# Optimization experiments

Measured on AMD Instinct MI355X. Metric: run time of the kernel, lower is better.

The kernel has to match this reference:

```python
import jax, jax.numpy as jnp
import numpy as np

WS = 7          # window size (square)
SS = 3          # shift size
NH = 6          # num heads
EPS = 1e-5      # LayerNorm eps (torch default)


def _ln(x, g, b):
    m = jnp.mean(x, axis=-1, keepdims=True)
    v = jnp.mean(jnp.square(x - m), axis=-1, keepdims=True)
    return (x - m) * jax.lax.rsqrt(v + EPS) * g + b


def _window_partition(x):
    # (B,H,W,C) -> (B*nW, WS*WS, C)
    B, H, W, C = x.shape
    x = x.reshape(B, H // WS, WS, W // WS, WS, C)
    return x.transpose(0, 1, 3, 2, 4, 5).reshape(-1, WS * WS, C)


def _window_reverse(w, B, H, W):
    C = w.shape[-1]
    x = w.reshape(B, H // WS, W // WS, WS, WS, C)
    return x.transpose(0, 1, 3, 2, 4, 5).reshape(B, H, W, C)


def _make_rpi():
    coords = np.stack(np.meshgrid(np.arange(WS), np.arange(WS), indexing='ij'))  # (2,WS,WS)
    cf = coords.reshape(2, -1)
    rel = cf[:, :, None] - cf[:, None, :]            # (2,N,N)
    rel = rel.transpose(1, 2, 0).astype(np.int64)
    rel[..., 0] += WS - 1
    rel[..., 1] += WS - 1
    rel[..., 0] *= 2 * WS - 1
    return rel.sum(-1)                               # (N,N)


def _make_mask(H, W):
    # standard shifted-window attention mask, values in {0, -100}
    img = np.zeros((H, W), dtype=np.float32)
    cnt = 0
    for hs in (slice(0, -WS), slice(-WS, -SS), slice(-SS, None)):
        for ws_ in (slice(0, -WS), slice(-WS, -SS), slice(-SS, None)):
            img[hs, ws_] = cnt
            cnt += 1
    win = img.reshape(H // WS, WS, W // WS, WS).transpose(0, 2, 1, 3).reshape(-1, WS * WS)
    diff = win[:, None, :] - win[:, :, None]
    return np.where(diff != 0, np.float32(-100.0), np.float32(0.0))  # (nW,N,N)


def setup_inputs() -> dict:
    key = jax.random.key(0)
    ks = jax.random.split(key, 8)
    B, H, W, C = 16, 112, 112, 192
    Dh = C * 4
    s = 0.02
    inp = {
        'x': jax.random.normal(ks[0], (B, H, W, C), jnp.float32),
        'mask_matrix': jnp.asarray(_make_mask(H, W)),
        'rpi': jnp.asarray(_make_rpi(), jnp.int32),
        'rpb_table': s * jax.random.normal(ks[1], ((2 * WS - 1) ** 2, NH), jnp.float32),
        'norm1_g': jnp.ones((C,), jnp.float32),
        'norm1_b': jnp.zeros((C,), jnp.float32),
        'qkv_w': s * jax.random.normal(ks[2], (3 * C, C), jnp.float32),
        'qkv_b': jnp.zeros((3 * C,), jnp.float32),
        'proj_w': s * jax.random.normal(ks[3], (C, C), jnp.float32),
        'proj_b': jnp.zeros((C,), jnp.float32),
        'norm2_g': jnp.ones((C,), jnp.float32),
        'norm2_b': jnp.zeros((C,), jnp.float32),
        'fc1_w': s * jax.random.normal(ks[4], (Dh, C), jnp.float32),
        'fc1_b': jnp.zeros((Dh,), jnp.float32),
        'fc2_w': s * jax.random.normal(ks[5], (C, Dh), jnp.float32),
        'fc2_b': jnp.zeros((C,), jnp.float32),
    }
    return inp


def reference(x, mask_matrix, rpi, rpb_table, norm1_g, norm1_b, qkv_w, qkv_b,
              proj_w, proj_b, norm2_g, norm2_b, fc1_w, fc1_b, fc2_w, fc2_b):
    B, H, W, C = x.shape
    N = WS * WS
    hd = C // NH
    scale = hd ** -0.5

    shortcut = x
    xn = _ln(x, norm1_g, norm1_b)
    shifted = jnp.roll(xn, shift=(-SS, -SS), axis=(1, 2))

    xw = _window_partition(shifted)                          # (B_, N, C)
    B_ = xw.shape[0]
    qkv = xw @ qkv_w.T + qkv_b                               # (B_, N, 3C)
    qkv = qkv.reshape(B_, N, 3, NH, hd).transpose(2, 0, 3, 1, 4)
    q, k, v = qkv[0] * scale, qkv[1], qkv[2]                 # (B_, NH, N, hd)

    attn = jnp.einsum('bhnd,bhmd->bhnm', q, k)               # (B_, NH, N, N)
    bias = rpb_table[rpi.reshape(-1)].reshape(N, N, NH).transpose(2, 0, 1)
    attn = attn + bias[None]

    nW = mask_matrix.shape[0]
    attn = attn.reshape(B_ // nW, nW, NH, N, N) + mask_matrix[None, :, None]
    attn = jax.nn.softmax(attn.reshape(B_, NH, N, N), axis=-1)

    out = jnp.einsum('bhnm,bhmd->bhnd', attn, v)             # (B_, NH, N, hd)
    out = out.transpose(0, 2, 1, 3).reshape(B_, N, C)
    out = out @ proj_w.T + proj_b

    shifted = _window_reverse(out, B, H, W)
    xa = jnp.roll(shifted, shift=(SS, SS), axis=(1, 2))
    x = shortcut + xa

    h = _ln(x, norm2_g, norm2_b)
    h = jax.nn.gelu(h @ fc1_w.T + fc1_b, approximate=False)
    h = h @ fc2_w.T + fc2_b
    return x + h
```

## Files before the change

### kernel.cpp

```cpp
#include <hip/hip_runtime.h>
#include <hip/hip_bf16.h>

typedef __hip_bfloat16 bf16;
typedef __attribute__((ext_vector_type(8))) short bh8;
typedef __attribute__((ext_vector_type(4))) short bh4;
typedef __attribute__((ext_vector_type(4))) float f4;

#define TOKENS 200704
#define CDIM   192

__device__ __forceinline__ void gload16(const bf16* g, bf16* l) {
    __builtin_amdgcn_global_load_lds((const __attribute__((address_space(1))) void*)g,
                                     (__attribute__((address_space(3))) void*)l,
                                     16, 0, 0);
}
#define MFMA __builtin_amdgcn_mfma_f32_16x16x32_bf16

__device__ __forceinline__ void stv(float* p, float v) { *p = v; }
__device__ __forceinline__ void stv(bf16* p, float v)  { *p = __float2bfloat16(v); }
__device__ __forceinline__ short f2bs(float v) {
    bf16 h = __float2bfloat16(v); return *(short*)&h;
}

__device__ __forceinline__ int row2tok(int row) {
    int win = row / 49, n = row - win * 49;
    int b = win >> 8, rem = win & 255;
    int hs = (rem >> 4) * 7 + n / 7;
    int wsx = (rem & 15) * 7 + n % 7;
    int hh = hs + 3; if (hh >= 112) hh -= 112;
    int ww = wsx + 3; if (ww >= 112) ww -= 112;
    return (b * 112 + hh) * 112 + ww;
}

__global__ void cvt_all(const float* __restrict__ a, const float* __restrict__ b,
                        const float* __restrict__ c, const float* __restrict__ d,
                        bf16* __restrict__ dst) {
    int i = blockIdx.x * 256 + threadIdx.x;
    if (i >= 442368) return;
    float v;
    if (i < 110592)       v = a[i];
    else if (i < 147456)  v = b[i - 110592];
    else if (i < 294912)  v = c[i - 147456];
    else                  v = d[i - 294912];
    dst[i] = __float2bfloat16(v);
}

__global__ void bmp_kernel(const int* __restrict__ rpi, const float* __restrict__ tab,
                           const float* __restrict__ mask, float* __restrict__ bmp) {
    int idx = blockIdx.x * 256 + threadIdx.x;
    if (idx >= 98304) return;
    int cls = idx / 24576, rem = idx - cls * 24576;
    int h = rem >> 12, qk = rem & 4095;
    int qq = qk >> 6, kk = qk & 63;
    float v;
    if (kk >= 49) v = -1e30f;
    else if (qq >= 49) v = 0.f;
    else {
        int rep = ((cls & 2) ? 240 : 0) + ((cls & 1) ? 15 : 0);
        v = tab[rpi[qq * 49 + kk] * 6 + h] + mask[rep * 2401 + qq * 49 + kk];
    }
    bmp[idx] = v;
}

template<int GATHER>
__global__ __launch_bounds__(256)
void ln_kernel(const float* __restrict__ src, const float* __restrict__ gw,
               const float* __restrict__ bw, bf16* __restrict__ dst) {
    const int lane = threadIdx.x & 63;
    const int gwv  = (blockIdx.x * 256 + threadIdx.x) >> 6;
    const int nwv  = (gridDim.x * 256) >> 6;
    const float g0 = gw[lane], g1 = gw[lane + 64], g2 = gw[lane + 128];
    const float b0 = bw[lane], b1 = bw[lane + 64], b2 = bw[lane + 128];
    for (int row = gwv; row < TOKENS; row += nwv) {
        const float* p = GATHER ? src + (size_t)row2tok(row) * CDIM
                                : src + (size_t)row * CDIM;
        float v0 = p[lane], v1 = p[lane + 64], v2 = p[lane + 128];
        float s = v0 + v1 + v2;
        float q = v0 * v0 + v1 * v1 + v2 * v2;
        #pragma unroll
        for (int o = 32; o; o >>= 1) { s += __shfl_xor(s, o, 64); q += __shfl_xor(q, o, 64); }
        float mean = s * (1.f / 192.f);
        float var  = q * (1.f / 192.f) - mean * mean;
        float rstd = rsqrtf(var + 1e-5f);
        bf16* d = dst + (size_t)row * CDIM;
        d[lane]       = __float2bfloat16((v0 - mean) * rstd * g0 + b0);
        d[lane + 64]  = __float2bfloat16((v1 - mean) * rstd * g1 + b1);
        d[lane + 128] = __float2bfloat16((v2 - mean) * rstd * g2 + b2);
    }
}

template<int EPI, int FUSELN, typename OutT>
__global__ __launch_bounds__(256)
void gemm_bt(const bf16* __restrict__ A, const bf16* __restrict__ W,
             const float* __restrict__ bias, OutT* out,
             const float* res, int N, int K,
             const float* __restrict__ g2, const float* __restrict__ b2g,
             bf16* __restrict__ hbuf) {
    __shared__ __align__(16) bf16 As[128 * 32];
    __shared__ __align__(16) bf16 Bs[192 * 32];
    __shared__ float rsum[FUSELN ? 128 : 1][2], rsq[FUSELN ? 128 : 1][2];
    const int tid = threadIdx.x, wid = tid >> 6, lane = tid & 63;
    const int mbase = blockIdx.y * 128, nbase = blockIdx.x * 192;
    const int wm = wid >> 1, wn = wid & 1;
    const int r = lane & 15, q = lane >> 4;
    const int sx = (q ^ ((r >> 1) & 3)) << 3;
    const bf16* Ab = A + (size_t)mbase * K;
    const bf16* Wb = W + (size_t)nbase * K;
    f4 acc[4][6] = {};
    const int cbase = wid * 64 + lane;
    for (int k0 = 0; k0 < K; k0 += 32) {
        #pragma unroll
        for (int p = 0; p < 2; ++p) {
            int ci = p * 256 + cbase;
            int row = ci >> 2, g = (ci & 3) ^ ((row >> 1) & 3);
            gload16(Ab + (size_t)row * K + (k0 + (g << 3)),
                    &As[(p * 256 + wid * 64) * 8]);
        }
        #pragma unroll
        for (int p = 0; p < 3; ++p) {
            int ci = p * 256 + cbase;
            int row = ci >> 2, g = (ci & 3) ^ ((row >> 1) & 3);
            gload16(Wb + (size_t)row * K + (k0 + (g << 3)),
                    &Bs[(p * 256 + wid * 64) * 8]);
        }
        __syncthreads();
        bh8 af[4], bfr[6];
        #pragma unroll
        for (int i = 0; i < 4; ++i)
            af[i] = *(const bh8*)&As[(wm * 64 + i * 16 + r) * 32 + sx];
        #pragma unroll
        for (int j = 0; j < 6; ++j)
            bfr[j] = *(const bh8*)&Bs[(wn * 96 + j * 16 + r) * 32 + sx];
        #pragma unroll
        for (int i = 0; i < 4; ++i)
            #pragma unroll
            for (int j = 0; j < 6; ++j)
                acc[i][j] = MFMA(af[i], bfr[j], acc[i][j], 0, 0, 0);
        __syncthreads();
    }
    const int cr = q, cc = r;
    if constexpr (EPI == 0) {
        #pragma unroll
        for (int i = 0; i < 4; ++i)
            #pragma unroll
            for (int j = 0; j < 6; ++j) {
                int ncol = nbase + wn * 96 + j * 16 + cc;
                float bv = bias[ncol];
                #pragma unroll
                for (int rr = 0; rr < 4; ++rr) {
                    int row = mbase + wm * 64 + i * 16 + cr * 4 + rr;
                    stv(&out[(size_t)row * N + ncol], acc[i][j][rr] + bv);
                }
            }
    } else {
        #pragma unroll
        for (int i = 0; i < 4; ++i) {
            size_t dstRow[4];
            float ps[4], pq[4];
            #pragma unroll
            for (int rr = 0; rr < 4; ++rr) {
                int row = mbase + wm * 64 + i * 16 + cr * 4 + rr;
                dstRow[rr] = (size_t)row2tok(row) * CDIM;
                ps[rr] = 0.f; pq[rr] = 0.f;
            }
            #pragma unroll
            for (int j = 0; j < 6; ++j) {
                int ncol = nbase + wn * 96 + j * 16 + cc;
                float bv = bias[ncol];
                #pragma unroll
                for (int rr = 0; rr < 4; ++rr) {
                    float v = acc[i][j][rr] + bv + res[dstRow[rr] + ncol];
                    stv(&out[dstRow[rr] + ncol], v);
                    acc[i][j][rr] = v;
                    ps[rr] += v; pq[rr] += v * v;
                }
            }
            if constexpr (FUSELN) {
                #pragma unroll
                for (int rr = 0; rr < 4; ++rr) {
                    float s = ps[rr], qq = pq[rr];
                    #pragma unroll
                    for (int o = 1; o < 16; o <<= 1) { s += __shfl_xor(s, o, 64); qq += __shfl_xor(qq, o, 64); }
                    if (cc == 0) {
                        int rl = wm * 64 + i * 16 + cr * 4 + rr;
                        rsum[rl][wn] = s; rsq[rl][wn] = qq;
                    }
                }
            }
        }
        if constexpr (FUSELN) {
            __syncthreads();
            #pragma unroll
            for (int i = 0; i < 4; ++i) {
                size_t dstRow[4];
                float mean[4], rstd[4];
                #pragma unroll
                for (int rr = 0; rr < 4; ++rr) {
                    int rl = wm * 64 + i * 16 + cr * 4 + rr;
                    dstRow[rr] = (size_t)row2tok(mbase + rl) * CDIM;
                    float m = (rsum[rl][0] + rsum[rl][1]) * (1.f / 192.f);
                    float var = (rsq[rl][0] + rsq[rl][1]) * (1.f / 192.f) - m * m;
                    mean[rr] = m; rstd[rr] = rsqrtf(var + 1e-5f);
                }
                #pragma unroll
                for (int j = 0; j < 6; ++j) {
                    int ncol = nbase + wn * 96 + j * 16 + cc;
                    float gv = g2[ncol], bvv = b2g[ncol];
                    #pragma unroll
                    for (int rr = 0; rr < 4; ++rr)
                        hbuf[dstRow[rr] + ncol] =
                            __float2bfloat16((acc[i][j][rr] - mean[rr]) * rstd[rr] * gv + bvv);
                }
            }
        }
    }
}

__global__ __launch_bounds__(384, 2)
void qkvattn_kernel(const bf16* __restrict__ xw, const bf16* __restrict__ wq,
                    const float* __restrict__ qkvb, const float* __restrict__ bmp,
                    bf16* __restrict__ attno) {
    __shared__ __align__(16) bf16 xsf[6][64][32];
    __shared__ __align__(16) bf16 qk[6][2][64][32];
    const int tid = threadIdx.x, h = tid >> 6, lane = tid & 63;
    const int r = lane & 15, q = lane >> 4;
    const int win = blockIdx.x;
    const int sxk = (q ^ ((r >> 1) & 3)) << 3;

    #pragma unroll
    for (int it = 0; it < 4; ++it) {
        int l = it * 384 + tid;
        int ks = l >> 8, rem = l & 255, tok = rem >> 2;
        int kg = (rem & 3) ^ ((tok >> 1) & 3);
        int srow = win * 49 + tok; if (srow > 200703) srow = 200703;
        gload16(xw + (size_t)srow * 192 + ks * 32 + kg * 8,
                &xsf[0][0][0] + (size_t)l * 8);
    }
    const bf16* wqh = wq + (size_t)(h * 32 + r) * 192 + q * 8;
    bh8 wqk[4], wv[2];
    #pragma unroll
    for (int i = 0; i < 4; ++i)
        wqk[i] = *(const bh8*)(wqh + (size_t)((i >> 1) * 192 + (i & 1) * 16) * 192);
    #pragma unroll
    for (int jv = 0; jv < 2; ++jv)
        wv[jv] = *(const bh8*)(wqh + (size_t)(384 + jv * 16) * 192);
    __syncthreads();
    f4 aqk[4][4] = {}, av[4][2] = {};
    #pragma unroll
    for (int ks = 0; ks < 6; ++ks) {
        bh8 nqk[4], nv[2];
        if (ks < 5) {
            #pragma unroll
            for (int i = 0; i < 4; ++i)
                nqk[i] = *(const bh8*)(wqh + (size_t)((i >> 1) * 192 + (i & 1) * 16) * 192 + (ks + 1) * 32);
            #pragma unroll
            for (int jv = 0; jv < 2; ++jv)
                nv[jv] = *(const bh8*)(wqh + (size_t)(384 + jv * 16) * 192 + (ks + 1) * 32);
        }
        bh8 xf[4];
        #pragma unroll
        for (int mt = 0; mt < 4; ++mt)
            xf[mt] = *(const bh8*)&xsf[ks][mt * 16 + r][sxk];
        #pragma unroll
        for (int i = 0; i < 4; ++i)
            #pragma unroll
            for (int jn = 0; jn < 4; ++jn)
                aqk[i][jn] = MFMA(wqk[i], xf[jn], aqk[i][jn], 0, 0, 0);
        #pragma unroll
        for (int mt = 0; mt < 4; ++mt)
            #pragma unroll
            for (int jv = 0; jv < 2; ++jv)
                av[mt][jv] = MFMA(xf[mt], wv[jv], av[mt][jv], 0, 0, 0);
        if (ks < 5) {
            #pragma unroll
            for (int i = 0; i < 4; ++i) wqk[i] = nqk[i];
            wv[0] = nv[0]; wv[1] = nv[1];
        }
    }
    __syncthreads();
    bf16* qkh = &qk[h][0][0][0];
    #pragma unroll
    for (int i = 0; i < 4; ++i) {
        const int t = i >> 1;
        const f4 bz = *(const f4*)&qkvb[t * 192 + h * 32 + (i & 1) * 16 + q * 4];
        const float sc = (i < 2) ? 0.17677669529663689f : 1.0f;
        #pragma unroll
        for (int jn = 0; jn < 4; ++jn) {
            const int tok = jn * 16 + r;
            bh4 w;
            #pragma unroll
            for (int rr = 0; rr < 4; ++rr)
                w[rr] = f2bs((aqk[i][jn][rr] + bz[rr]) * sc);
            const int g = (((i & 1) * 4 + q) ^ ((tok & 3) << 1));
            *(bh4*)&qkh[(t * 64 + tok) * 32 + g * 4] = w;
        }
    }
    bf16* vth = &xsf[0][0][0] + h * 2048;
    #pragma unroll
    for (int jv = 0; jv < 2; ++jv) {
        const float bv = qkvb[384 + h * 32 + jv * 16 + r];
        const int d = jv * 16 + r;
        #pragma unroll
        for (int mt = 0; mt < 4; ++mt) {
            bh4 w;
            #pragma unroll
            for (int rr = 0; rr < 4; ++rr)
                w[rr] = f2bs(av[mt][jv][rr] + bv);
            const int g = ((mt * 4 + q) ^ ((r & 7) << 1));
            *(bh4*)&vth[d * 64 + g * 4] = w;
        }
    }
    f4 as[4][4] = {};
    {
        const int sl = ((2 * q) ^ ((r & 3) << 1)) << 2;
        bh8 kf[4], qf[4];
        #pragma unroll
        for (int mt = 0; mt < 4; ++mt)
            kf[mt] = *(const bh8*)&qkh[(64 + mt * 16 + r) * 32 + sl];
        #pragma unroll
        for (int jn = 0; jn < 4; ++jn)
            qf[jn] = *(const bh8*)&qkh[(jn * 16 + r) * 32 + sl];
        #pragma unroll
        for (int mt = 0; mt < 4; ++mt)
            #pragma unroll
            for (int jn = 0; jn < 4; ++jn)
                as[mt][jn] = MFMA(kf[mt], qf[jn], as[mt][jn], 0, 0, 0);
    }
    const int rem = win & 255;
    const int cls = (((rem >> 4) == 15) ? 2 : 0) + (((rem & 15) == 15) ? 1 : 0);
    const float* bmh = bmp + ((size_t)(cls * 6 + h) << 12);
    #pragma unroll
    for (int jn = 0; jn < 4; ++jn) {
        const int qq = jn * 16 + r;
        #pragma unroll
        for (int mt = 0; mt < 4; ++mt) {
            const f4 b = *(const f4*)&bmh[qq * 64 + mt * 16 + q * 4];
            #pragma unroll
            for (int rr = 0; rr < 4; ++rr) as[mt][jn][rr] += b[rr];
        }
    }
    float inv4[4];
    #pragma unroll
    for (int jn = 0; jn < 4; ++jn) {
        float mx = -1e30f;
        #pragma unroll
        for (int mt = 0; mt < 4; ++mt)
            #pragma unroll
            for (int rr = 0; rr < 4; ++rr) mx = fmaxf(mx, as[mt][jn][rr]);
        mx = fmaxf(mx, __shfl_xor(mx, 16, 64));
        mx = fmaxf(mx, __shfl_xor(mx, 32, 64));
        float sm = 0.f;
        #pragma unroll
        for (int mt = 0; mt < 4; ++mt)
            #pragma unroll
            for (int rr = 0; rr < 4; ++rr) {
                float e = __expf(as[mt][jn][rr] - mx);
                as[mt][jn][rr] = e; sm += e;
            }
        sm += __shfl_xor(sm, 16, 64);
        sm += __shfl_xor(sm, 32, 64);
        inv4[jn] = __builtin_amdgcn_rcpf(sm);
    }
    #pragma unroll
    for (int jn = 0; jn < 4; ++jn) {
        const int qq = jn * 16 + r;
        #pragma unroll
        for (int mt = 0; mt < 4; ++mt) {
            bh4 w;
            #pragma unroll
            for (int rr = 0; rr < 4; ++rr) w[rr] = f2bs(as[mt][jn][rr] * inv4[jn]);
            const int g = ((mt * 4 + q) ^ ((r & 7) << 1));
            *(bh4*)&qkh[qq * 64 + g * 4] = w;
        }
    }
    f4 ao[4][2] = {};
    #pragma unroll
    for (int k2 = 0; k2 < 2; ++k2) {
        const int sl = ((k2 * 8 + 2 * q) ^ ((r & 7) << 1)) << 2;
        bh8 pf[4], vf[2];
        #pragma unroll
        for (int mt = 0; mt < 4; ++mt)
            pf[mt] = *(const bh8*)&qkh[(mt * 16 + r) * 64 + sl];
        #pragma unroll
        for (int jv = 0; jv < 2; ++jv)
            vf[jv] = *(const bh8*)&vth[(jv * 16 + r) * 64 + sl];
        #pragma unroll
        for (int mt = 0; mt < 4; ++mt)
            #pragma unroll
            for (int jv = 0; jv < 2; ++jv)
                ao[mt][jv] = MFMA(pf[mt], vf[jv], ao[mt][jv], 0, 0, 0);
    }
    #pragma unroll
    for (int mt = 0; mt < 4; ++mt)
        #pragma unroll
        for (int jv = 0; jv < 2; ++jv) {
            const int d = jv * 16 + r;
            #pragma unroll
            for (int rr = 0; rr < 4; ++rr) {
                const int qq = mt * 16 + q * 4 + rr;
                if (qq < 49)
                    attno[((size_t)win * 49 + qq) * 192 + h * 32 + d] =
                        __float2bfloat16(ao[mt][jv][rr]);
            }
        }
}

__global__ __launch_bounds__(256, 4)
void mlp_kernel(const bf16* __restrict__ Aht, const bf16* __restrict__ w1,
                const float* __restrict__ b1, const bf16* __restrict__ w2,
                const float* __restrict__ b2, float* __restrict__ out) {
    __shared__ __align__(16) bf16 As[6][64][32];
    __shared__ __align__(16) bf16 Hs[2][64][64];
    const int tid = threadIdx.x, wid = tid >> 6, lane = tid & 63;
    const int mbase = blockIdx.x * 64;
    const int r = lane & 15, q = lane >> 4, ko = q * 8;
    const int sxA = (q ^ ((r >> 1) & 3)) << 3;
    #pragma unroll
    for (int it = 0; it < 6; ++it) {
        int l = it * 256 + wid * 64 + lane;
        int ks = l >> 8, rem2 = l & 255, row = rem2 >> 2;
        int g = (rem2 & 3) ^ ((row >> 1) & 3);
        gload16(Aht + (size_t)(mbase + row) * 192 + ks * 32 + g * 8,
                &As[0][0][0] + (size_t)(it * 256 + wid * 64) * 8);
    }
    __syncthreads();
    f4 acc2[4][3] = {};
    for (int c = 0; c < 12; ++c) {
        const int cb = c * 64;
        bh8 w1f[6];
        #pragma unroll
        for (int ks = 0; ks < 6; ++ks)
            w1f[ks] = *(const bh8*)&w1[(size_t)(cb + wid * 16 + r) * 192 + ks * 32 + ko];
        f4 acc1[4] = {};
        #pragma unroll
        for (int ks = 0; ks < 6; ++ks)
            #pragma unroll
            for (int i = 0; i < 4; ++i) {
                bh8 af = *(const bh8*)(&As[ks][0][0] + (i * 16 + r) * 32 + sxA);
                acc1[i] = MFMA(af, w1f[ks], acc1[i], 0, 0, 0);
            }
        bh8 w2f[2][3];
        #pragma unroll
        for (int k2 = 0; k2 < 2; ++k2)
            #pragma unroll
            for (int j = 0; j < 3; ++j)
                w2f[k2][j] = *(const bh8*)&w2[(size_t)(wid * 48 + j * 16 + r) * 768 + cb + k2 * 32 + ko];
        const float b1v = b1[cb + wid * 16 + r];
        bf16 (*Hp)[64] = Hs[c & 1];
        #pragma unroll
        for (int i = 0; i < 4; ++i) {
            #pragma unroll
            for (int rr = 0; rr < 4; ++rr) {
                int row = i * 16 + q * 4 + rr;
                int col = wid * 16 + r;
                float v = acc1[i][rr] + b1v;
                float u = v * (1.5957691216f + 0.0713548162f * v * v);
                float en = __expf(-u);
                float t = __builtin_amdgcn_rcpf(1.f + en);
                Hp[row][(((col >> 3) ^ (row & 7)) << 3) | (col & 7)] =
                    __float2bfloat16(v * t);
            }
        }
        __syncthreads();
        #pragma unroll
        for (int k2 = 0; k2 < 2; ++k2)
            #pragma unroll
            for (int i = 0; i < 4; ++i) {
                int row = i * 16 + r;
                bh8 af = *(const bh8*)(&Hp[row][0] + ((((k2 * 4 + q) ^ (row & 7)) & 7) << 3));
                #pragma unroll
                for (int j = 0; j < 3; ++j)
                    acc2[i][j] = MFMA(af, w2f[k2][j], acc2[i][j], 0, 0, 0);
            }
    }
    #pragma unroll
    for (int i = 0; i < 4; ++i)
        #pragma unroll
        for (int j = 0; j < 3; ++j) {
            int ncol = wid * 48 + j * 16 + r;
            float bv = b2[ncol];
            #pragma unroll
            for (int rr = 0; rr < 4; ++rr) {
                size_t idx = (size_t)(mbase + i * 16 + q * 4 + rr) * 192 + ncol;
                out[idx] = acc2[i][j][rr] + bv + out[idx];
            }
        }
}

extern "C" void kernel_launch(void* const* d_in, const int* in_sizes, int n_in,
                              void* d_out, int out_size, void* d_ws, size_t ws_size,
                              hipStream_t stream) {
    const float* x     = (const float*)d_in[0];
    const float* mask  = (const float*)d_in[1];
    const int*   rpi   = (const int*)d_in[2];
    const float* rpb   = (const float*)d_in[3];
    const float* n1g   = (const float*)d_in[4];
    const float* n1b   = (const float*)d_in[5];
    const float* qkvw  = (const float*)d_in[6];
    const float* qkvb  = (const float*)d_in[7];
    const float* projw = (const float*)d_in[8];
    const float* projb = (const float*)d_in[9];
    const float* n2g   = (const float*)d_in[10];
    const float* n2b   = (const float*)d_in[11];
    const float* fc1w  = (const float*)d_in[12];
    const float* fc1b  = (const float*)d_in[13];
    const float* fc2w  = (const float*)d_in[14];
    const float* fc2b  = (const float*)d_in[15];

    char* ws = (char*)d_ws;
    bf16*  attno  = (bf16*)ws;
    float* bmp    = (float*)(ws + 77070336);
    bf16*  wq     = (bf16*)(ws + 77463552);
    bf16*  wp     = (bf16*)(ws + 77684736);
    bf16*  w1     = (bf16*)(ws + 77758464);
    bf16*  w2     = (bf16*)(ws + 78053376);
    bf16*  xw     = (bf16*)d_out;
    float* x1     = (float*)d_out;

    const bool fuse = ws_size >= 155418624ull;
    bf16* hbuf = fuse ? (bf16*)(ws + 78348288) : (bf16*)ws;

    cvt_all<<<1728, 256, 0, stream>>>(qkvw, projw, fc1w, fc2w, wq);
    bmp_kernel<<<384, 256, 0, stream>>>(rpi, rpb, mask, bmp);

    ln_kernel<1><<<2048, 256, 0, stream>>>(x, n1g, n1b, xw);
    qkvattn_kernel<<<4096, 384, 0, stream>>>(xw, wq, qkvb, bmp, attno);
    if (fuse) {
        gemm_bt<1, 1, float><<<dim3(1, 1568), 256, 0, stream>>>(
            attno, wp, projb, x1, x, 192, 192, n2g, n2b, hbuf);
    } else {
        gemm_bt<1, 0, float><<<dim3(1, 1568), 256, 0, stream>>>(
            attno, wp, projb, x1, x, 192, 192, nullptr, nullptr, nullptr);
        ln_kernel<0><<<2048, 256, 0, stream>>>(x1, n2g, n2b, hbuf);
    }
    mlp_kernel<<<3136, 256, 0, stream>>>(hbuf, w1, fc1b, w2, fc2b, (float*)d_out);
}
```

Measured before the change: 722.1 us.

## Fuse projection, residual, LayerNorm2 and MLP into a single kernel

Merges the projection GEMM with residual add, the second LayerNorm and the MLP into one kernel that keeps the projected rows in registers and LDS. The normalized activations are written back into the shared A buffer and consumed directly by the fc1/fc2 stages, and the final output is scattered to token order with the residual added. This removes the global round trips for the intermediate fp32 residual and bf16 normalized buffer, plus two kernel launches. In exchange, occupancy is lowered to 3 blocks per SM and projection weights are read from global per warp.

```diff
diff --git a/kernel.cpp b/kernel.cpp
--- a/kernel.cpp
+++ b/kernel.cpp
@@ -16,8 +16,6 @@
 }
 #define MFMA __builtin_amdgcn_mfma_f32_16x16x32_bf16
 
-__device__ __forceinline__ void stv(float* p, float v) { *p = v; }
-__device__ __forceinline__ void stv(bf16* p, float v)  { *p = __float2bfloat16(v); }
 __device__ __forceinline__ short f2bs(float v) {
     bf16 h = __float2bfloat16(v); return *(short*)&h;
 }
@@ -62,7 +60,6 @@
     bmp[idx] = v;
 }
 
-template<int GATHER>
 __global__ __launch_bounds__(256)
 void ln_kernel(const float* __restrict__ src, const float* __restrict__ gw,
                const float* __restrict__ bw, bf16* __restrict__ dst) {
@@ -72,8 +69,7 @@
     const float g0 = gw[lane], g1 = gw[lane + 64], g2 = gw[lane + 128];
     const float b0 = bw[lane], b1 = bw[lane + 64], b2 = bw[lane + 128];
     for (int row = gwv; row < TOKENS; row += nwv) {
-        const float* p = GATHER ? src + (size_t)row2tok(row) * CDIM
-                                : src + (size_t)row * CDIM;
+        const float* p = src + (size_t)row2tok(row) * CDIM;
         float v0 = p[lane], v1 = p[lane + 64], v2 = p[lane + 128];
         float s = v0 + v1 + v2;
         float q = v0 * v0 + v1 * v1 + v2 * v2;
@@ -86,133 +82,6 @@
         d[lane]       = __float2bfloat16((v0 - mean) * rstd * g0 + b0);
         d[lane + 64]  = __float2bfloat16((v1 - mean) * rstd * g1 + b1);
         d[lane + 128] = __float2bfloat16((v2 - mean) * rstd * g2 + b2);
-    }
-}
-
-template<int EPI, int FUSELN, typename OutT>
-__global__ __launch_bounds__(256)
-void gemm_bt(const bf16* __restrict__ A, const bf16* __restrict__ W,
-             const float* __restrict__ bias, OutT* out,
-             const float* res, int N, int K,
-             const float* __restrict__ g2, const float* __restrict__ b2g,
-             bf16* __restrict__ hbuf) {
-    __shared__ __align__(16) bf16 As[128 * 32];
-    __shared__ __align__(16) bf16 Bs[192 * 32];
-    __shared__ float rsum[FUSELN ? 128 : 1][2], rsq[FUSELN ? 128 : 1][2];
-    const int tid = threadIdx.x, wid = tid >> 6, lane = tid & 63;
-    const int mbase = blockIdx.y * 128, nbase = blockIdx.x * 192;
-    const int wm = wid >> 1, wn = wid & 1;
-    const int r = lane & 15, q = lane >> 4;
-    const int sx = (q ^ ((r >> 1) & 3)) << 3;
-    const bf16* Ab = A + (size_t)mbase * K;
-    const bf16* Wb = W + (size_t)nbase * K;
-    f4 acc[4][6] = {};
-    const int cbase = wid * 64 + lane;
-    for (int k0 = 0; k0 < K; k0 += 32) {
-        #pragma unroll
-        for (int p = 0; p < 2; ++p) {
-            int ci = p * 256 + cbase;
-            int row = ci >> 2, g = (ci & 3) ^ ((row >> 1) & 3);
-            gload16(Ab + (size_t)row * K + (k0 + (g << 3)),
-                    &As[(p * 256 + wid * 64) * 8]);
-        }
-        #pragma unroll
-        for (int p = 0; p < 3; ++p) {
-            int ci = p * 256 + cbase;
-            int row = ci >> 2, g = (ci & 3) ^ ((row >> 1) & 3);
-            gload16(Wb + (size_t)row * K + (k0 + (g << 3)),
-                    &Bs[(p * 256 + wid * 64) * 8]);
-        }
-        __syncthreads();
-        bh8 af[4], bfr[6];
-        #pragma unroll
-        for (int i = 0; i < 4; ++i)
-            af[i] = *(const bh8*)&As[(wm * 64 + i * 16 + r) * 32 + sx];
-        #pragma unroll
-        for (int j = 0; j < 6; ++j)
-            bfr[j] = *(const bh8*)&Bs[(wn * 96 + j * 16 + r) * 32 + sx];
-        #pragma unroll
-        for (int i = 0; i < 4; ++i)
-            #pragma unroll
-            for (int j = 0; j < 6; ++j)
-                acc[i][j] = MFMA(af[i], bfr[j], acc[i][j], 0, 0, 0);
-        __syncthreads();
-    }
-    const int cr = q, cc = r;
-    if constexpr (EPI == 0) {
-        #pragma unroll
-        for (int i = 0; i < 4; ++i)
-            #pragma unroll
-            for (int j = 0; j < 6; ++j) {
-                int ncol = nbase + wn * 96 + j * 16 + cc;
-                float bv = bias[ncol];
-                #pragma unroll
-                for (int rr = 0; rr < 4; ++rr) {
-                    int row = mbase + wm * 64 + i * 16 + cr * 4 + rr;
-                    stv(&out[(size_t)row * N + ncol], acc[i][j][rr] + bv);
-                }
-            }
-    } else {
-        #pragma unroll
-        for (int i = 0; i < 4; ++i) {
-            size_t dstRow[4];
-            float ps[4], pq[4];
-            #pragma unroll
-            for (int rr = 0; rr < 4; ++rr) {
-                int row = mbase + wm * 64 + i * 16 + cr * 4 + rr;
-                dstRow[rr] = (size_t)row2tok(row) * CDIM;
-                ps[rr] = 0.f; pq[rr] = 0.f;
-            }
-            #pragma unroll
-            for (int j = 0; j < 6; ++j) {
-                int ncol = nbase + wn * 96 + j * 16 + cc;
-                float bv = bias[ncol];
-                #pragma unroll
-                for (int rr = 0; rr < 4; ++rr) {
-                    float v = acc[i][j][rr] + bv + res[dstRow[rr] + ncol];
-                    stv(&out[dstRow[rr] + ncol], v);
-                    acc[i][j][rr] = v;
-                    ps[rr] += v; pq[rr] += v * v;
-                }
-            }
-            if constexpr (FUSELN) {
-                #pragma unroll
-                for (int rr = 0; rr < 4; ++rr) {
-                    float s = ps[rr], qq = pq[rr];
-                    #pragma unroll
-                    for (int o = 1; o < 16; o <<= 1) { s += __shfl_xor(s, o, 64); qq += __shfl_xor(qq, o, 64); }
-                    if (cc == 0) {
-                        int rl = wm * 64 + i * 16 + cr * 4 + rr;
-                        rsum[rl][wn] = s; rsq[rl][wn] = qq;
-                    }
-                }
-            }
-        }
-        if constexpr (FUSELN) {
-            __syncthreads();
-            #pragma unroll
-            for (int i = 0; i < 4; ++i) {
-                size_t dstRow[4];
-                float mean[4], rstd[4];
-                #pragma unroll
-                for (int rr = 0; rr < 4; ++rr) {
-                    int rl = wm * 64 + i * 16 + cr * 4 + rr;
-                    dstRow[rr] = (size_t)row2tok(mbase + rl) * CDIM;
-                    float m = (rsum[rl][0] + rsum[rl][1]) * (1.f / 192.f);
-                    float var = (rsq[rl][0] + rsq[rl][1]) * (1.f / 192.f) - m * m;
-                    mean[rr] = m; rstd[rr] = rsqrtf(var + 1e-5f);
-                }
-                #pragma unroll
-                for (int j = 0; j < 6; ++j) {
-                    int ncol = nbase + wn * 96 + j * 16 + cc;
-                    float gv = g2[ncol], bvv = b2g[ncol];
-                    #pragma unroll
-                    for (int rr = 0; rr < 4; ++rr)
-                        hbuf[dstRow[rr] + ncol] =
-                            __float2bfloat16((acc[i][j][rr] - mean[rr]) * rstd[rr] * gv + bvv);
-                }
-            }
-        }
     }
 }
 
@@ -405,23 +274,100 @@
         }
 }
 
-__global__ __launch_bounds__(256, 4)
-void mlp_kernel(const bf16* __restrict__ Aht, const bf16* __restrict__ w1,
-                const float* __restrict__ b1, const bf16* __restrict__ w2,
-                const float* __restrict__ b2, float* __restrict__ out) {
+__global__ __launch_bounds__(256, 3)
+void projmlp_kernel(const bf16* __restrict__ attno, const bf16* __restrict__ wp,
+                    const float* __restrict__ projb, const float* __restrict__ xres,
+                    const float* __restrict__ g2, const float* __restrict__ b2g,
+                    const bf16* __restrict__ w1, const float* __restrict__ b1,
+                    const bf16* __restrict__ w2, const float* __restrict__ b2,
+                    float* __restrict__ out) {
     __shared__ __align__(16) bf16 As[6][64][32];
     __shared__ __align__(16) bf16 Hs[2][64][64];
+    __shared__ float rsum[64][4], rsq[64][4], mr[64][2];
     const int tid = threadIdx.x, wid = tid >> 6, lane = tid & 63;
     const int mbase = blockIdx.x * 64;
     const int r = lane & 15, q = lane >> 4, ko = q * 8;
     const int sxA = (q ^ ((r >> 1) & 3)) << 3;
+    bf16* As0 = &As[0][0][0];
     #pragma unroll
     for (int it = 0; it < 6; ++it) {
         int l = it * 256 + wid * 64 + lane;
         int ks = l >> 8, rem2 = l & 255, row = rem2 >> 2;
         int g = (rem2 & 3) ^ ((row >> 1) & 3);
-        gload16(Aht + (size_t)(mbase + row) * 192 + ks * 32 + g * 8,
-                &As[0][0][0] + (size_t)(it * 256 + wid * 64) * 8);
+        gload16(attno + (size_t)(mbase + row) * 192 + ks * 32 + g * 8,
+                As0 + (size_t)(it * 256 + wid * 64) * 8);
+    }
+    __syncthreads();
+    f4 pacc[4][3] = {};
+    #pragma unroll
+    for (int ks = 0; ks < 6; ++ks) {
+        bh8 wpf[3];
+        #pragma unroll
+        for (int j = 0; j < 3; ++j)
+            wpf[j] = *(const bh8*)&wp[(size_t)(wid * 48 + j * 16 + r) * 192 + ks * 32 + ko];
+        #pragma unroll
+        for (int i = 0; i < 4; ++i) {
+            bh8 af = *(const bh8*)(As0 + ks * 2048 + (i * 16 + r) * 32 + sxA);
+            #pragma unroll
+            for (int j = 0; j < 3; ++j)
+                pacc[i][j] = MFMA(af, wpf[j], pacc[i][j], 0, 0, 0);
+        }
+    }
+    float pbv[3];
+    #pragma unroll
+    for (int j = 0; j < 3; ++j) pbv[j] = projb[wid * 48 + j * 16 + r];
+    #pragma unroll
+    for (int i = 0; i < 4; ++i) {
+        int tok[4];
+        float ps[4] = {}, pq2[4] = {};
+        #pragma unroll
+        for (int rr = 0; rr < 4; ++rr)
+            tok[rr] = row2tok(mbase + i * 16 + q * 4 + rr);
+        #pragma unroll
+        for (int j = 0; j < 3; ++j) {
+            const int col = wid * 48 + j * 16 + r;
+            #pragma unroll
+            for (int rr = 0; rr < 4; ++rr) {
+                float v = pacc[i][j][rr] + pbv[j] + xres[(size_t)tok[rr] * 192 + col];
+                pacc[i][j][rr] = v;
+                ps[rr] += v; pq2[rr] += v * v;
+            }
+        }
+        #pragma unroll
+        for (int rr = 0; rr < 4; ++rr) {
+            float s = ps[rr], qq = pq2[rr];
+            #pragma unroll
+            for (int o = 1; o < 16; o <<= 1) { s += __shfl_xor(s, o, 64); qq += __shfl_xor(qq, o, 64); }
+            if (r == 0) {
+                const int row = i * 16 + q * 4 + rr;
+                rsum[row][wid] = s; rsq[row][wid] = qq;
+            }
+        }
+    }
+    __syncthreads();
+    if (tid < 64) {
+        float s = 0.f, qq = 0.f;
+        #pragma unroll
+        for (int w = 0; w < 4; ++w) { s += rsum[tid][w]; qq += rsq[tid][w]; }
+        float m = s * (1.f / 192.f);
+        float var = qq * (1.f / 192.f) - m * m;
+        mr[tid][0] = m; mr[tid][1] = rsqrtf(var + 1e-5f);
+    }
+    __syncthreads();
+    #pragma unroll
+    for (int j = 0; j < 3; ++j) {
+        const int col = wid * 48 + j * 16 + r;
+        const float gv = g2[col], bvv = b2g[col];
+        const int ks2 = col >> 5, w32 = col & 31;
+        #pragma unroll
+        for (int i = 0; i < 4; ++i)
+            #pragma unroll
+            for (int rr = 0; rr < 4; ++rr) {
+                const int row = i * 16 + q * 4 + rr;
+                float hv = (pacc[i][j][rr] - mr[row][0]) * mr[row][1] * gv + bvv;
+                const int slot8 = (w32 >> 3) ^ ((row >> 1) & 3);
+                As0[ks2 * 2048 + row * 32 + slot8 * 8 + (w32 & 7)] = __float2bfloat16(hv);
+            }
     }
     __syncthreads();
     f4 acc2[4][3] = {};
@@ -436,7 +382,7 @@
         for (int ks = 0; ks < 6; ++ks)
             #pragma unroll
             for (int i = 0; i < 4; ++i) {
-                bh8 af = *(const bh8*)(&As[ks][0][0] + (i * 16 + r) * 32 + sxA);
+                bh8 af = *(const bh8*)(As0 + ks * 2048 + (i * 16 + r) * 32 + sxA);
                 acc1[i] = MFMA(af, w1f[ks], acc1[i], 0, 0, 0);
             }
         bh8 w2f[2][3];
@@ -474,17 +420,20 @@
             }
     }
     #pragma unroll
-    for (int i = 0; i < 4; ++i)
+    for (int i = 0; i < 4; ++i) {
+        int tok[4];
+        #pragma unroll
+        for (int rr = 0; rr < 4; ++rr)
+            tok[rr] = row2tok(mbase + i * 16 + q * 4 + rr);
         #pragma unroll
         for (int j = 0; j < 3; ++j) {
             int ncol = wid * 48 + j * 16 + r;
             float bv = b2[ncol];
             #pragma unroll
-            for (int rr = 0; rr < 4; ++rr) {
-                size_t idx = (size_t)(mbase + i * 16 + q * 4 + rr) * 192 + ncol;
-                out[idx] = acc2[i][j][rr] + bv + out[idx];
-            }
-        }
+            for (int rr = 0; rr < 4; ++rr)
+                out[(size_t)tok[rr] * 192 + ncol] = pacc[i][j][rr] + acc2[i][j][rr] + bv;
+        }
+    }
 }
 
 extern "C" void kernel_launch(void* const* d_in, const int* in_sizes, int n_in,
@@ -515,23 +464,12 @@
     bf16*  w1     = (bf16*)(ws + 77758464);
     bf16*  w2     = (bf16*)(ws + 78053376);
     bf16*  xw     = (bf16*)d_out;
-    float* x1     = (float*)d_out;
-
-    const bool fuse = ws_size >= 155418624ull;
-    bf16* hbuf = fuse ? (bf16*)(ws + 78348288) : (bf16*)ws;
 
     cvt_all<<<1728, 256, 0, stream>>>(qkvw, projw, fc1w, fc2w, wq);
     bmp_kernel<<<384, 256, 0, stream>>>(rpi, rpb, mask, bmp);
 
-    ln_kernel<1><<<2048, 256, 0, stream>>>(x, n1g, n1b, xw);
+    ln_kernel<<<2048, 256, 0, stream>>>(x, n1g, n1b, xw);
     qkvattn_kernel<<<4096, 384, 0, stream>>>(xw, wq, qkvb, bmp, attno);
-    if (fuse) {
-        gemm_bt<1, 1, float><<<dim3(1, 1568), 256, 0, stream>>>(
-            attno, wp, projb, x1, x, 192, 192, n2g, n2b, hbuf);
-    } else {
-        gemm_bt<1, 0, float><<<dim3(1, 1568), 256, 0, stream>>>(
-            attno, wp, projb, x1, x, 192, 192, nullptr, nullptr, nullptr);
-        ln_kernel<0><<<2048, 256, 0, stream>>>(x1, n2g, n2b, hbuf);
-    }
-    mlp_kernel<<<3136, 256, 0, stream>>>(hbuf, w1, fc1b, w2, fc2b, (float*)d_out);
-}
+    projmlp_kernel<<<3136, 256, 0, stream>>>(attno, wp, projb, x, n2g, n2b,
+                                             w1, fc1b, w2, fc2b, (float*)d_out);
+}
```

Measured after the change: 596.4 us (median of 2 runs). 17.4% less time.
